# Kernel optimization log

Hardware: AMD Instinct MI355X
Metric: run time of the kernel (lower is better)

Reference implementation:

```python
import jax, jax.numpy as jnp
import numpy as np

B, D, S = 128, 256, 512
K, H, NCLS = 50, 256, 2
THRES = 0.3  # conceptshap threshold


def _l2norm(x, axis):
    n = jnp.sqrt(jnp.sum(x * x, axis=axis, keepdims=True))
    return x / jnp.maximum(n, 1e-12)


def setup_inputs() -> dict:
    key = jax.random.key(0)
    ks = jax.random.split(key, 6)
    return {
        "f_input": jax.random.normal(ks[0], (B, D, S), dtype=jnp.float32),
        "targets": jax.random.uniform(ks[1], (B,), dtype=jnp.float32),
        "topic_vector": jax.random.uniform(ks[2], (D, K), minval=-0.5, maxval=0.5, dtype=jnp.float32),
        "rec_vector_1": jax.random.uniform(ks[3], (K, H), minval=-0.5, maxval=0.5, dtype=jnp.float32),
        "rec_vector_2": jax.random.uniform(ks[4], (H, D), minval=-0.5, maxval=0.5, dtype=jnp.float32),
        "Wc": jax.random.normal(ks[5], (D, NCLS), dtype=jnp.float32) * 0.05,
        "bc": jnp.zeros((NCLS,), dtype=jnp.float32),
        "causal": 0,
    }


def reference(f_input, targets, topic_vector, rec_vector_1, rec_vector_2, Wc, bc, causal):
    # text path (n=3), model_name != 'transformer' -> swap to [B, S, D]
    x = jnp.swapaxes(f_input, 1, 2)                # [B, S, D]
    x_n = _l2norm(x, axis=-1)                      # F.normalize(dim=n-1)
    tv_n = _l2norm(topic_vector, axis=0)           # [D, K], column-normalized

    topic_prob = jnp.einsum('bsd,dk->bsk', x, tv_n)      # [B, S, K]
    topic_prob_n = jnp.einsum('bsd,dk->bsk', x_n, tv_n)  # [B, S, K]

    # conceptshap: no softmax, hard threshold mask
    mask = (topic_prob_n > THRES).astype(topic_prob.dtype)
    topic_prob_am = topic_prob * mask
    topic_prob_sum = jnp.sum(topic_prob_am, axis=-1, keepdims=True) + 0.001
    topic_prob_nn = topic_prob_am / (topic_prob_sum + 1e-8)

    rec_layer_1 = jax.nn.relu(jnp.einsum('bsk,kh->bsh', topic_prob_nn, rec_vector_1))
    rec_layer_2 = jnp.einsum('bsh,hd->bsd', rec_layer_1, rec_vector_2)  # [B, S, D]

    ae_loss = jnp.mean((x_n - rec_layer_2) ** 2)

    rec_out = jnp.swapaxes(rec_layer_2, 1, 2)      # back to [B, D, S]
    # frozen classifier: mean over seq + linear head
    pred = jnp.mean(rec_out, axis=-1) @ Wc + bc    # [B, NCLS]

    # concept_sim: mean of per-concept top-(B//4) similarity scores, negated
    res = topic_prob_n.reshape(-1, K).T            # [K, B*S]
    topv, _ = jax.lax.top_k(res, B // 4)
    concept_sim = -jnp.mean(topv)

    concept_far = jnp.mean(tv_n.T @ tv_n - jnp.eye(K, dtype=tv_n.dtype))

    return (pred, jnp.float32(0.0), concept_sim, concept_far, topic_prob_nn, ae_loss)
```

## Files before the change

### kernel.cpp

```cpp
#include <hip/hip_runtime.h>
#include <math.h>

#define BB 128
#define DD 256
#define SS 512
#define KK 50
#define HH 256
#define TS 128
#define NTILES (BB * SS / TS)
#define NBLK (NTILES * 2)
#define BS (BB * SS)

#define CHUNK 1024
#define NCH (BS / CHUNK)
#define NCHBLK (KK * NCH / 4)
#define TOPK 32
#define MAXSURV 512
#define NSUB (TS / 16)

#define TVN_OFF 0
#define TVNT_OFF (TVN_OFF + DD * KK)
#define TPNT_OFF (TVNT_OFF + KK * DD)
#define PREDACC_OFF (TPNT_OFF + KK * BS)
#define AE_OFF (PREDACC_OFF + BB * DD)
#define SIM_OFF (AE_OFF + 1)
#define CNT_OFF (AE_OFF + 2)
#define SIMD_OFF (AE_OFF + 3)
#define TFLAG_OFF (AE_OFF + 4)
#define TCNT_OFF (TFLAG_OFF + NTILES)
#define NZERO (BB * DD + 4 + 2 * NTILES)
#define LIST_OFF (TCNT_OFF + NTILES)
#define CAND_OFF (LIST_OFF + MAXSURV)

#define OUT_NN_OFF 259
#define OUT_AE_IDX (OUT_NN_OFF + KK * BS)

__device__ __forceinline__ unsigned fkey(float f) {
  unsigned u = __float_as_uint(f);
  return (u & 0x80000000u) ? ~u : (u | 0x80000000u);
}
__device__ __forceinline__ float keyval(unsigned T) {
  unsigned u = (T & 0x80000000u) ? (T & 0x7FFFFFFFu) : ~T;
  return __uint_as_float(u);
}

__global__ __launch_bounds__(256) void tvn_kernel(const float* __restrict__ tv,
                                                  float* __restrict__ tvn,
                                                  float* __restrict__ tvnT,
                                                  float* __restrict__ zbase) {
  __shared__ float red[256];
  const int k = blockIdx.x, t = threadIdx.x;
  {
    const int gid = k * 256 + t;
    for (int i = gid; i < NZERO; i += KK * 256) zbase[i] = 0.0f;
  }
  float v = tv[t * KK + k];
  red[t] = v * v;
  __syncthreads();
  for (int off = 128; off > 0; off >>= 1) {
    if (t < off) red[t] += red[t + off];
    __syncthreads();
  }
  float inv = 1.0f / fmaxf(sqrtf(red[0]), 1e-12f);
  const float nv = v * inv;
  tvn[t * KK + k] = nv;
  tvnT[k * DD + t] = nv;
}

__global__ __launch_bounds__(256, 4) void main_kernel(
    const float* __restrict__ f_input, const float* __restrict__ tvnT,
    float* __restrict__ out_nn, float* __restrict__ tpn_t,
    float* __restrict__ ae_acc, int* __restrict__ surv_cnt,
    int* __restrict__ surv_list, int* __restrict__ tile_flag,
    int* __restrict__ tile_cnt) {
  __shared__ int wflag[4];
  __shared__ int decision;

  const int blk = blockIdx.x;
  const int tile = blk >> 1;
  const int half = blk & 1;
  const int b = tile >> 2;
  const int s0 = (tile & 3) * TS;
  const int t = threadIdx.x;
  const int lane = t & 63;
  const int wid = t >> 6;
  const int kb = __builtin_amdgcn_readfirstlane(half * 4 + wid);

  const float* tvk[7];
  bool kval[7];
  #pragma unroll
  for (int j = 0; j < 7; ++j) {
    const int k = kb + 8 * j;
    kval[j] = (k < KK);
    tvk[j] = tvnT + (size_t)(kval[j] ? k : (KK - 1)) * DD;
  }

  const float* xp = f_input + (size_t)b * DD * SS + s0 + 2 * lane;

  float acc0[7], acc1[7];
  #pragma unroll
  for (int j = 0; j < 7; ++j) { acc0[j] = 0.0f; acc1[j] = 0.0f; }

  float2 xb[2][4];
  #pragma unroll
  for (int i = 0; i < 4; ++i) xb[0][i] = *(const float2*)(xp + (size_t)i * SS);

  float s2_0 = 0.0f, s2_1 = 0.0f;
  int buf = 0;
  for (int part = 0; part < 8; ++part) {
    float p0 = 0.0f, p1 = 0.0f;
    #pragma unroll
    for (int dd = 0; dd < 32; dd += 4) {
      const int d0 = part * 32 + dd;
      const int dn = (d0 + 4 < DD) ? (d0 + 4) : 0;
      #pragma unroll
      for (int i = 0; i < 4; ++i) xb[buf ^ 1][i] = *(const float2*)(xp + (size_t)(dn + i) * SS);
      const float2 xa = xb[buf][0], xc2 = xb[buf][1], xc3 = xb[buf][2], xc4 = xb[buf][3];
      p0 += xa.x * xa.x; p0 += xc2.x * xc2.x; p0 += xc3.x * xc3.x; p0 += xc4.x * xc4.x;
      p1 += xa.y * xa.y; p1 += xc2.y * xc2.y; p1 += xc3.y * xc3.y; p1 += xc4.y * xc4.y;
      #pragma unroll
      for (int j = 0; j < 7; ++j) {
        const float4 tq = *(const float4*)(tvk[j] + d0);
        acc0[j] += xa.x * tq.x; acc0[j] += xc2.x * tq.y;
        acc0[j] += xc3.x * tq.z; acc0[j] += xc4.x * tq.w;
        acc1[j] += xa.y * tq.x; acc1[j] += xc2.y * tq.y;
        acc1[j] += xc3.y * tq.z; acc1[j] += xc4.y * tq.w;
      }
      buf ^= 1;
    }
    s2_0 = (part == 0) ? p0 : (s2_0 + p0);
    s2_1 = (part == 0) ? p1 : (s2_1 + p1);
  }
  const float i0 = 1.0f / fmaxf(sqrtf(s2_0), 1e-12f);
  const float i1 = 1.0f / fmaxf(sqrtf(s2_1), 1e-12f);

  bool m = false;
  const size_t gs = (size_t)b * SS + s0 + 2 * lane;
  #pragma unroll
  for (int j = 0; j < 7; ++j) {
    if (kval[j]) {
      const int k = kb + 8 * j;
      float2 o;
      o.x = acc0[j] * i0;
      o.y = acc1[j] * i1;
      *(float2*)(tpn_t + (size_t)k * BS + gs) = o;
      m = m | (o.x > 0.3f) | (o.y > 0.3f);
    }
  }

  const int w = __any((int)m);
  if (lane == 0) wflag[wid] = w;
  __syncthreads();
  const int blockAny = wflag[0] | wflag[1] | wflag[2] | wflag[3];

  if (t == 0) {
    const int old = atomicOr(&tile_flag[tile], blockAny);
    const int done = atomicAdd(&tile_cnt[tile], 1);
    int dec = 0;
    if (done == 1) {
      const int fl = old | blockAny;
      if (fl) {
        const int idx = atomicAdd(surv_cnt, 1);
        if (idx < MAXSURV) surv_list[idx] = tile;
      } else {
        atomicAdd(ae_acc, (float)TS);
        dec = 1;
      }
    }
    decision = dec;
  }
  __syncthreads();
  if (decision) {
    float* ob = out_nn + ((size_t)b * SS + s0) * KK;
    for (int p2 = t; p2 < TS * KK; p2 += 256) ob[p2] = 0.0f;
  }
}

__global__ __launch_bounds__(256) void chunk_surv_kernel(
    const float* __restrict__ tpn_t, float* __restrict__ cand,
    const float* __restrict__ f_input, const float* __restrict__ rec1,
    const float* __restrict__ rec2, const int* __restrict__ surv_cnt,
    const int* __restrict__ surv_list, float* __restrict__ out_nn,
    float* __restrict__ predacc, float* __restrict__ ae_acc) {
  __shared__ __align__(16) float NNk[KK * 20];
  __shared__ __align__(16) float R1t[HH * 20];
  __shared__ float nprt[16][17];
  __shared__ float nrm[16], invn[16];
  __shared__ float pm[8 * DD];
  __shared__ float red4[4];

  const int t = threadIdx.x;
  const int lane = t & 63, wid = t >> 6;

  if (blockIdx.x < NCHBLK) {
    const int gchunk = blockIdx.x * 4 + wid;
    const int k = gchunk >> 6;
    const int c = gchunk & (NCH - 1);
    const float* row = tpn_t + (size_t)k * BS + c * CHUNK;

    float v[16];
    unsigned key[16];
    #pragma unroll
    for (int j = 0; j < 16; ++j) {
      v[j] = row[lane + j * 64];
      key[j] = fkey(v[j]);
    }
    unsigned T = 0;
    for (int bit = 31; bit >= 0; --bit) {
      const unsigned ct = T | (1u << bit);
      int cnt = 0;
      #pragma unroll
      for (int j = 0; j < 16; ++j) cnt += (key[j] >= ct) ? 1 : 0;
      #pragma unroll
      for (int off = 1; off < 64; off <<= 1) cnt += __shfl_xor(cnt, off);
      if (cnt >= TOPK) T = ct;
    }
    int cg = 0;
    #pragma unroll
    for (int j = 0; j < 16; ++j) cg += (key[j] > T) ? 1 : 0;
    int incl = cg;
    #pragma unroll
    for (int off = 1; off < 64; off <<= 1) {
      int y = __shfl_up(incl, off);
      if (lane >= off) incl += y;
    }
    const int excl = incl - cg;
    const int total_gt = __shfl(incl, 63);

    float* cb = cand + (size_t)gchunk * TOPK;
    int pos = excl;
    #pragma unroll
    for (int j = 0; j < 16; ++j) {
      if (key[j] > T) cb[pos++] = v[j];
    }
    if (lane < TOPK - total_gt) cb[total_gt + lane] = keyval(T);
    return;
  }

  const int bid = blockIdx.x - NCHBLK;
  int cnt = *surv_cnt;
  if (cnt > MAXSURV) cnt = MAXSURV;
  const int ntask = NSUB * cnt;

  for (int task = bid; task < ntask; task += 64) {
    const int tile = surv_list[task / NSUB];
    const int q = task % NSUB;
    const int b = tile >> 2;
    const int s0 = (tile & 3) * TS + q * 16;
    const float* fb = f_input + (size_t)b * DD * SS;
    const size_t gs0 = (size_t)b * SS + s0;

    for (int p = t; p < KK * 16; p += 256) {
      const int k = p >> 4, ss = p & 15;
      NNk[k * 20 + ss] = tpn_t[(size_t)k * BS + gs0 + ss];
    }
    {
      const int ss = t & 15, part = t >> 4;
      const float* xc = fb + (size_t)(part * 16) * SS + s0 + ss;
      float p = 0.0f;
      #pragma unroll
      for (int i = 0; i < 16; ++i) {
        const float v = xc[(size_t)i * SS];
        p += v * v;
      }
      nprt[part][ss] = p;
    }
    __syncthreads();
    if (t < 16) {
      float s2 = 0.0f;
      #pragma unroll
      for (int i = 0; i < 16; ++i) s2 += nprt[i][t];
      const float n = fmaxf(sqrtf(s2), 1e-12f);
      nrm[t] = n;
      invn[t] = 1.0f / n;
      float sm = 0.0f;
      for (int k = 0; k < KK; ++k) {
        const float tpn = NNk[k * 20 + t];
        sm += (tpn > 0.3f) ? tpn * n : 0.0f;
      }
      const float idv = 1.0f / (sm + 0.001f + 1e-8f);
      for (int k = 0; k < KK; ++k) {
        const float tpn = NNk[k * 20 + t];
        NNk[k * 20 + t] = (tpn > 0.3f) ? tpn * n * idv : 0.0f;
      }
    }
    __syncthreads();

    for (int p = t; p < 16 * KK; p += 256) {
      const int ss = p / KK, k = p - ss * KK;
      out_nn[(gs0 + ss) * KK + k] = NNk[k * 20 + ss];
    }

    {
      float a[16];
      #pragma unroll
      for (int i = 0; i < 16; ++i) a[i] = 0.0f;
      #pragma unroll 2
      for (int k = 0; k < KK; ++k) {
        const float r = rec1[k * HH + t];
        const float4* np = (const float4*)&NNk[k * 20];
        #pragma unroll
        for (int qq = 0; qq < 4; ++qq) {
          const float4 nv = np[qq];
          a[qq * 4 + 0] += nv.x * r;
          a[qq * 4 + 1] += nv.y * r;
          a[qq * 4 + 2] += nv.z * r;
          a[qq * 4 + 3] += nv.w * r;
        }
      }
      #pragma unroll
      for (int i = 0; i < 16; ++i) R1t[t * 20 + i] = fmaxf(a[i], 0.0f);
    }
    __syncthreads();

    const int tx = t & 31, ty = t >> 5;
    const int d0 = tx * 8, sb = ty * 2;
    float c2[2][8];
    #pragma unroll
    for (int i = 0; i < 2; ++i)
      #pragma unroll
      for (int j = 0; j < 8; ++j) c2[i][j] = 0.0f;
    for (int h0 = 0; h0 < HH; h0 += 8) {
      float4 B0[8], B1[8];
      #pragma unroll
      for (int u = 0; u < 8; ++u) {
        B0[u] = *(const float4*)(rec2 + (h0 + u) * DD + d0);
        B1[u] = *(const float4*)(rec2 + (h0 + u) * DD + d0 + 4);
      }
      #pragma unroll
      for (int u = 0; u < 8; ++u) {
        const float2 a01 = *(const float2*)(&R1t[(h0 + u) * 20 + sb]);
        const float bv[8] = {B0[u].x, B0[u].y, B0[u].z, B0[u].w,
                             B1[u].x, B1[u].y, B1[u].z, B1[u].w};
        #pragma unroll
        for (int j = 0; j < 8; ++j) {
          c2[0][j] += a01.x * bv[j];
          c2[1][j] += a01.y * bv[j];
        }
      }
    }
    #pragma unroll
    for (int j = 0; j < 8; ++j) pm[ty * DD + d0 + j] = c2[0][j] + c2[1][j];
    __syncthreads();
    {
      float sum = 0.0f;
      #pragma unroll
      for (int r = 0; r < 8; ++r) sum += pm[r * DD + t];
      atomicAdd(&predacc[(size_t)b * DD + t], sum);
    }
    float e = 0.0f;
    #pragma unroll
    for (int j = 0; j < 8; ++j) {
      #pragma unroll
      for (int i = 0; i < 2; ++i) {
        const float x = fb[(size_t)(d0 + j) * SS + s0 + sb + i];
        const float diff = x * invn[sb + i] - c2[i][j];
        e += diff * diff;
      }
    }
    #pragma unroll
    for (int off = 1; off < 64; off <<= 1) e += __shfl_xor(e, off);
    if (lane == 0) red4[wid] = e;
    __syncthreads();
    if (t == 0) atomicAdd(ae_acc, red4[0] + red4[1] + red4[2] + red4[3]);
    __syncthreads();
  }
}

__global__ __launch_bounds__(256) void merge_finalize_kernel(
    const float* __restrict__ cand, const float* __restrict__ predacc,
    const float* __restrict__ Wc, const float* __restrict__ bc,
    const float* __restrict__ ae_acc, float* __restrict__ sim_acc,
    unsigned* __restrict__ sim_done, const float* __restrict__ tvn,
    float* __restrict__ out) {
  __shared__ float r0[256], r1[256];
  const int blk = blockIdx.x;
  const int t = threadIdx.x;

  if (blk >= BB) {
    if (t < 64) {
      const int k = blk - BB;
      const int lane = t;
      const float* row = cand + (size_t)k * (NCH * TOPK);
      float v[32];
      unsigned key[32];
      #pragma unroll
      for (int j = 0; j < 32; ++j) {
        v[j] = row[lane + j * 64];
        key[j] = fkey(v[j]);
      }
      unsigned T = 0;
      for (int bit = 31; bit >= 0; --bit) {
        const unsigned ct = T | (1u << bit);
        int cnt = 0;
        #pragma unroll
        for (int j = 0; j < 32; ++j) cnt += (key[j] >= ct) ? 1 : 0;
        #pragma unroll
        for (int off = 1; off < 64; off <<= 1) cnt += __shfl_xor(cnt, off);
        if (cnt >= TOPK) T = ct;
      }
      float s = 0.0f;
      int cgt = 0;
      #pragma unroll
      for (int j = 0; j < 32; ++j) {
        if (key[j] > T) { s += v[j]; cgt++; }
      }
      #pragma unroll
      for (int off = 1; off < 64; off <<= 1) {
        s += __shfl_xor(s, off);
        cgt += __shfl_xor(cgt, off);
      }
      if (lane == 0) {
        atomicAdd(sim_acc, s + (float)(TOPK - cgt) * keyval(T));
        __threadfence();
        const unsigned c = atomicAdd(sim_done, 1u);
        if (c == KK - 1) {
          __threadfence();
          const float tot = atomicAdd(sim_acc, 0.0f);
          out[257] = -tot * (1.0f / (float)(KK * TOPK));
        }
      }
    }
    return;
  }

  const float s = predacc[(size_t)blk * DD + t];
  r0[t] = s * Wc[t * 2 + 0];
  r1[t] = s * Wc[t * 2 + 1];
  __syncthreads();
  for (int off = 128; off > 0; off >>= 1) {
    if (t < off) { r0[t] += r0[t + off]; r1[t] += r1[t + off]; }
    __syncthreads();
  }
  if (t == 0) {
    out[blk * 2 + 0] = r0[0] * (1.0f / (float)SS) + bc[0];
    out[blk * 2 + 1] = r1[0] * (1.0f / (float)SS) + bc[1];
    if (blk == 0) {
      out[256] = 0.0f;
      out[OUT_AE_IDX] = (*ae_acc) * (1.0f / ((float)BB * (float)SS * (float)DD));
    }
  }
  if (blk == 0) {
    __syncthreads();
    float rs = 0.0f;
    for (int k = 0; k < KK; ++k) rs += tvn[t * KK + k];
    r0[t] = rs * rs;
    __syncthreads();
    for (int off = 128; off > 0; off >>= 1) {
      if (t < off) r0[t] += r0[t + off];
      __syncthreads();
    }
    if (t == 0) out[258] = (r0[0] - (float)KK) / ((float)KK * (float)KK);
  }
}

extern "C" void kernel_launch(void* const* d_in, const int* in_sizes, int n_in,
                              void* d_out, int out_size, void* d_ws, size_t ws_size,
                              hipStream_t stream) {
  (void)in_sizes; (void)n_in; (void)out_size; (void)ws_size;
  const float* f_input = (const float*)d_in[0];
  const float* tv = (const float*)d_in[2];
  const float* rec1 = (const float*)d_in[3];
  const float* rec2 = (const float*)d_in[4];
  const float* Wc = (const float*)d_in[5];
  const float* bc = (const float*)d_in[6];

  float* out = (float*)d_out;
  float* ws = (float*)d_ws;
  float* tvn = ws + TVN_OFF;
  float* tvnT = ws + TVNT_OFF;
  float* tpn_t = ws + TPNT_OFF;
  float* predacc = ws + PREDACC_OFF;
  float* ae_acc = ws + AE_OFF;
  float* sim_acc = ws + SIM_OFF;
  int* surv_cnt = (int*)(ws + CNT_OFF);
  unsigned* sim_done = (unsigned*)(ws + SIMD_OFF);
  int* tile_flag = (int*)(ws + TFLAG_OFF);
  int* tile_cnt = (int*)(ws + TCNT_OFF);
  int* surv_list = (int*)(ws + LIST_OFF);
  float* cand = ws + CAND_OFF;

  tvn_kernel<<<KK, 256, 0, stream>>>(tv, tvn, tvnT, predacc);
  main_kernel<<<NBLK, 256, 0, stream>>>(f_input, tvnT, out + OUT_NN_OFF, tpn_t,
                                        ae_acc, surv_cnt, surv_list,
                                        tile_flag, tile_cnt);
  chunk_surv_kernel<<<NCHBLK + 64, 256, 0, stream>>>(
      tpn_t, cand, f_input, rec1, rec2, surv_cnt, surv_list,
      out + OUT_NN_OFF, predacc, ae_acc);
  merge_finalize_kernel<<<BB + KK, 256, 0, stream>>>(
      cand, predacc, Wc, bc, ae_acc, sim_acc, sim_done, tvn, out);
}
```

Baseline: 225.8 us.

## Fuse four kernel launches into one cooperative kernel with grid syncs

```diff
diff --git a/kernel.cpp b/kernel.cpp
--- a/kernel.cpp
+++ b/kernel.cpp
@@ -1,4 +1,5 @@
 #include <hip/hip_runtime.h>
+#include <hip/hip_cooperative_groups.h>
 #include <math.h>
 
 #define BB 128
@@ -44,6 +45,423 @@
   return __uint_as_float(u);
 }
 
+union __align__(16) AllShared {
+  float red[512];
+  struct { int wflag[4]; int decision; } mn;
+  struct {
+    float NNk[KK * 20];
+    float R1t[HH * 20];
+    float nprt[16][17];
+    float nrm[16];
+    float invn[16];
+    float pm[8 * DD];
+    float red4[4];
+  } sv;
+};
+
+__global__ __launch_bounds__(256, 4) void fused_kernel(
+    const float* __restrict__ f_input, const float* __restrict__ tv,
+    const float* __restrict__ rec1, const float* __restrict__ rec2,
+    const float* __restrict__ Wc, const float* __restrict__ bc,
+    float* __restrict__ out, float* __restrict__ ws) {
+  __shared__ AllShared sh;
+
+  float* tvn = ws + TVN_OFF;
+  float* tvnT = ws + TVNT_OFF;
+  float* tpn_t = ws + TPNT_OFF;
+  float* predacc = ws + PREDACC_OFF;
+  float* ae_acc = ws + AE_OFF;
+  float* sim_acc = ws + SIM_OFF;
+  int* surv_cnt = (int*)(ws + CNT_OFF);
+  unsigned* sim_done = (unsigned*)(ws + SIMD_OFF);
+  int* tile_flag = (int*)(ws + TFLAG_OFF);
+  int* tile_cnt = (int*)(ws + TCNT_OFF);
+  int* surv_list = (int*)(ws + LIST_OFF);
+  float* cand = ws + CAND_OFF;
+  float* out_nn = out + OUT_NN_OFF;
+
+  const int t = threadIdx.x;
+  const int lane = t & 63, wid = t >> 6;
+
+  {
+    const int gid = blockIdx.x * 256 + t;
+    if (gid < NZERO) predacc[gid] = 0.0f;
+    if (blockIdx.x < KK) {
+      const int k = blockIdx.x;
+      float v = tv[t * KK + k];
+      sh.red[t] = v * v;
+      __syncthreads();
+      for (int off = 128; off > 0; off >>= 1) {
+        if (t < off) sh.red[t] += sh.red[t + off];
+        __syncthreads();
+      }
+      const float inv = 1.0f / fmaxf(sqrtf(sh.red[0]), 1e-12f);
+      const float nv = v * inv;
+      tvn[t * KK + k] = nv;
+      tvnT[k * DD + t] = nv;
+    }
+  }
+  cooperative_groups::this_grid().sync();
+
+  {
+    const int blk = blockIdx.x;
+    const int tile = blk >> 1;
+    const int half = blk & 1;
+    const int b = tile >> 2;
+    const int s0 = (tile & 3) * TS;
+    const int kb = __builtin_amdgcn_readfirstlane(half * 4 + wid);
+
+    const float* tvk[7];
+    bool kval[7];
+    #pragma unroll
+    for (int j = 0; j < 7; ++j) {
+      const int k = kb + 8 * j;
+      kval[j] = (k < KK);
+      tvk[j] = tvnT + (size_t)(kval[j] ? k : (KK - 1)) * DD;
+    }
+
+    const float* xp = f_input + (size_t)b * DD * SS + s0 + 2 * lane;
+
+    float acc0[7], acc1[7];
+    #pragma unroll
+    for (int j = 0; j < 7; ++j) { acc0[j] = 0.0f; acc1[j] = 0.0f; }
+
+    float2 xb[2][8];
+    #pragma unroll
+    for (int i = 0; i < 8; ++i) xb[0][i] = *(const float2*)(xp + (size_t)i * SS);
+
+    float s2_0 = 0.0f, s2_1 = 0.0f;
+    int buf = 0;
+    for (int part = 0; part < 8; ++part) {
+      float p0 = 0.0f, p1 = 0.0f;
+      #pragma unroll
+      for (int dd = 0; dd < 32; dd += 8) {
+        const int d0 = part * 32 + dd;
+        const int dn = (d0 + 8 < DD) ? (d0 + 8) : 0;
+        #pragma unroll
+        for (int i = 0; i < 8; ++i) xb[buf ^ 1][i] = *(const float2*)(xp + (size_t)(dn + i) * SS);
+        #pragma unroll
+        for (int g = 0; g < 2; ++g) {
+          const float2 xa = xb[buf][4 * g + 0], xc2 = xb[buf][4 * g + 1],
+                       xc3 = xb[buf][4 * g + 2], xc4 = xb[buf][4 * g + 3];
+          p0 += xa.x * xa.x; p0 += xc2.x * xc2.x; p0 += xc3.x * xc3.x; p0 += xc4.x * xc4.x;
+          p1 += xa.y * xa.y; p1 += xc2.y * xc2.y; p1 += xc3.y * xc3.y; p1 += xc4.y * xc4.y;
+          #pragma unroll
+          for (int j = 0; j < 7; ++j) {
+            const float4 tq = *(const float4*)(tvk[j] + d0 + 4 * g);
+            acc0[j] += xa.x * tq.x; acc0[j] += xc2.x * tq.y;
+            acc0[j] += xc3.x * tq.z; acc0[j] += xc4.x * tq.w;
+            acc1[j] += xa.y * tq.x; acc1[j] += xc2.y * tq.y;
+            acc1[j] += xc3.y * tq.z; acc1[j] += xc4.y * tq.w;
+          }
+        }
+        buf ^= 1;
+      }
+      s2_0 = (part == 0) ? p0 : (s2_0 + p0);
+      s2_1 = (part == 0) ? p1 : (s2_1 + p1);
+    }
+    const float i0 = 1.0f / fmaxf(sqrtf(s2_0), 1e-12f);
+    const float i1 = 1.0f / fmaxf(sqrtf(s2_1), 1e-12f);
+
+    bool m = false;
+    const size_t gs = (size_t)b * SS + s0 + 2 * lane;
+    #pragma unroll
+    for (int j = 0; j < 7; ++j) {
+      if (kval[j]) {
+        const int k = kb + 8 * j;
+        float2 o;
+        o.x = acc0[j] * i0;
+        o.y = acc1[j] * i1;
+        *(float2*)(tpn_t + (size_t)k * BS + gs) = o;
+        m = m | (o.x > 0.3f) | (o.y > 0.3f);
+      }
+    }
+
+    const int w = __any((int)m);
+    if (lane == 0) sh.mn.wflag[wid] = w;
+    __syncthreads();
+    const int blockAny = sh.mn.wflag[0] | sh.mn.wflag[1] | sh.mn.wflag[2] | sh.mn.wflag[3];
+
+    if (t == 0) {
+      const int old = atomicOr(&tile_flag[tile], blockAny);
+      const int done = atomicAdd(&tile_cnt[tile], 1);
+      int dec = 0;
+      if (done == 1) {
+        const int fl = old | blockAny;
+        if (fl) {
+          const int idx = atomicAdd(surv_cnt, 1);
+          if (idx < MAXSURV) surv_list[idx] = tile;
+        } else {
+          atomicAdd(ae_acc, (float)TS);
+          dec = 1;
+        }
+      }
+      sh.mn.decision = dec;
+    }
+    __syncthreads();
+    if (sh.mn.decision) {
+      float* ob = out_nn + ((size_t)b * SS + s0) * KK;
+      for (int p2 = t; p2 < TS * KK; p2 += 256) ob[p2] = 0.0f;
+    }
+  }
+  cooperative_groups::this_grid().sync();
+
+  if (blockIdx.x < NCHBLK) {
+    const int gchunk = blockIdx.x * 4 + wid;
+    const int k = gchunk >> 6;
+    const int c = gchunk & (NCH - 1);
+    const float* row = tpn_t + (size_t)k * BS + c * CHUNK;
+
+    float v[16];
+    unsigned key[16];
+    #pragma unroll
+    for (int j = 0; j < 16; ++j) {
+      v[j] = row[lane + j * 64];
+      key[j] = fkey(v[j]);
+    }
+    unsigned T = 0;
+    for (int bit = 31; bit >= 0; --bit) {
+      const unsigned ct = T | (1u << bit);
+      int cnt = 0;
+      #pragma unroll
+      for (int j = 0; j < 16; ++j) cnt += (key[j] >= ct) ? 1 : 0;
+      #pragma unroll
+      for (int off = 1; off < 64; off <<= 1) cnt += __shfl_xor(cnt, off);
+      if (cnt >= TOPK) T = ct;
+    }
+    int cge = 0;
+    #pragma unroll
+    for (int j = 0; j < 16; ++j) cge += (key[j] > T) ? 1 : 0;
+    int incl = cge;
+    #pragma unroll
+    for (int off = 1; off < 64; off <<= 1) {
+      int y = __shfl_up(incl, off);
+      if (lane >= off) incl += y;
+    }
+    const int excl = incl - cge;
+    const int total_gt = __shfl(incl, 63);
+
+    float* cb = cand + (size_t)gchunk * TOPK;
+    int pos = excl;
+    #pragma unroll
+    for (int j = 0; j < 16; ++j) {
+      if (key[j] > T) cb[pos++] = v[j];
+    }
+    if (lane < TOPK - total_gt) cb[total_gt + lane] = keyval(T);
+  } else if (blockIdx.x < NCHBLK + 64) {
+    float* NNk = sh.sv.NNk;
+    float* R1t = sh.sv.R1t;
+    const int bid = blockIdx.x - NCHBLK;
+    int cnt = *surv_cnt;
+    if (cnt > MAXSURV) cnt = MAXSURV;
+    const int ntask = NSUB * cnt;
+
+    for (int task = bid; task < ntask; task += 64) {
+      const int tile = surv_list[task / NSUB];
+      const int q = task % NSUB;
+      const int b = tile >> 2;
+      const int s0 = (tile & 3) * TS + q * 16;
+      const float* fb = f_input + (size_t)b * DD * SS;
+      const size_t gs0 = (size_t)b * SS + s0;
+
+      for (int p = t; p < KK * 16; p += 256) {
+        const int k = p >> 4, ss = p & 15;
+        NNk[k * 20 + ss] = tpn_t[(size_t)k * BS + gs0 + ss];
+      }
+      {
+        const int ss = t & 15, part = t >> 4;
+        const float* xc = fb + (size_t)(part * 16) * SS + s0 + ss;
+        float p = 0.0f;
+        #pragma unroll
+        for (int i = 0; i < 16; ++i) {
+          const float v = xc[(size_t)i * SS];
+          p += v * v;
+        }
+        sh.sv.nprt[part][ss] = p;
+      }
+      __syncthreads();
+      if (t < 16) {
+        float s2 = 0.0f;
+        #pragma unroll
+        for (int i = 0; i < 16; ++i) s2 += sh.sv.nprt[i][t];
+        const float n = fmaxf(sqrtf(s2), 1e-12f);
+        sh.sv.nrm[t] = n;
+        sh.sv.invn[t] = 1.0f / n;
+        float sm = 0.0f;
+        for (int k = 0; k < KK; ++k) {
+          const float tpn = NNk[k * 20 + t];
+          sm += (tpn > 0.3f) ? tpn * n : 0.0f;
+        }
+        const float idv = 1.0f / (sm + 0.001f + 1e-8f);
+        for (int k = 0; k < KK; ++k) {
+          const float tpn = NNk[k * 20 + t];
+          NNk[k * 20 + t] = (tpn > 0.3f) ? tpn * n * idv : 0.0f;
+        }
+      }
+      __syncthreads();
+
+      for (int p = t; p < 16 * KK; p += 256) {
+        const int ss = p / KK, k = p - ss * KK;
+        out_nn[(gs0 + ss) * KK + k] = NNk[k * 20 + ss];
+      }
+
+      {
+        float a[16];
+        #pragma unroll
+        for (int i = 0; i < 16; ++i) a[i] = 0.0f;
+        #pragma unroll 2
+        for (int k = 0; k < KK; ++k) {
+          const float r = rec1[k * HH + t];
+          const float4* np = (const float4*)&NNk[k * 20];
+          #pragma unroll
+          for (int qq = 0; qq < 4; ++qq) {
+            const float4 nv = np[qq];
+            a[qq * 4 + 0] += nv.x * r;
+            a[qq * 4 + 1] += nv.y * r;
+            a[qq * 4 + 2] += nv.z * r;
+            a[qq * 4 + 3] += nv.w * r;
+          }
+        }
+        #pragma unroll
+        for (int i = 0; i < 16; ++i) R1t[t * 20 + i] = fmaxf(a[i], 0.0f);
+      }
+      __syncthreads();
+
+      const int tx = t & 31, ty = t >> 5;
+      const int d0 = tx * 8, sb = ty * 2;
+      float c2[2][8];
+      #pragma unroll
+      for (int i = 0; i < 2; ++i)
+        #pragma unroll
+        for (int j = 0; j < 8; ++j) c2[i][j] = 0.0f;
+      for (int h0 = 0; h0 < HH; h0 += 8) {
+        float4 B0[8], B1[8];
+        #pragma unroll
+        for (int u = 0; u < 8; ++u) {
+          B0[u] = *(const float4*)(rec2 + (h0 + u) * DD + d0);
+          B1[u] = *(const float4*)(rec2 + (h0 + u) * DD + d0 + 4);
+        }
+        #pragma unroll
+        for (int u = 0; u < 8; ++u) {
+          const float2 a01 = *(const float2*)(&R1t[(h0 + u) * 20 + sb]);
+          const float bv[8] = {B0[u].x, B0[u].y, B0[u].z, B0[u].w,
+                               B1[u].x, B1[u].y, B1[u].z, B1[u].w};
+          #pragma unroll
+          for (int j = 0; j < 8; ++j) {
+            c2[0][j] += a01.x * bv[j];
+            c2[1][j] += a01.y * bv[j];
+          }
+        }
+      }
+      #pragma unroll
+      for (int j = 0; j < 8; ++j) sh.sv.pm[ty * DD + d0 + j] = c2[0][j] + c2[1][j];
+      __syncthreads();
+      {
+        float sum = 0.0f;
+        #pragma unroll
+        for (int r = 0; r < 8; ++r) sum += sh.sv.pm[r * DD + t];
+        atomicAdd(&predacc[(size_t)b * DD + t], sum);
+      }
+      float e = 0.0f;
+      #pragma unroll
+      for (int j = 0; j < 8; ++j) {
+        #pragma unroll
+        for (int i = 0; i < 2; ++i) {
+          const float x = fb[(size_t)(d0 + j) * SS + s0 + sb + i];
+          const float diff = x * sh.sv.invn[sb + i] - c2[i][j];
+          e += diff * diff;
+        }
+      }
+      #pragma unroll
+      for (int off = 1; off < 64; off <<= 1) e += __shfl_xor(e, off);
+      if (lane == 0) sh.sv.red4[wid] = e;
+      __syncthreads();
+      if (t == 0) atomicAdd(ae_acc, sh.sv.red4[0] + sh.sv.red4[1] + sh.sv.red4[2] + sh.sv.red4[3]);
+      __syncthreads();
+    }
+  }
+  cooperative_groups::this_grid().sync();
+
+  {
+    const int blk = blockIdx.x;
+    if (blk >= BB && blk < BB + KK) {
+      if (t < 64) {
+        const int k = blk - BB;
+        const float* row = cand + (size_t)k * (NCH * TOPK);
+        float v[32];
+        unsigned key[32];
+        #pragma unroll
+        for (int j = 0; j < 32; ++j) {
+          v[j] = row[t + j * 64];
+          key[j] = fkey(v[j]);
+        }
+        unsigned T = 0;
+        for (int bit = 31; bit >= 0; --bit) {
+          const unsigned ct = T | (1u << bit);
+          int cnt = 0;
+          #pragma unroll
+          for (int j = 0; j < 32; ++j) cnt += (key[j] >= ct) ? 1 : 0;
+          #pragma unroll
+          for (int off = 1; off < 64; off <<= 1) cnt += __shfl_xor(cnt, off);
+          if (cnt >= TOPK) T = ct;
+        }
+        float s = 0.0f;
+        int cgt = 0;
+        #pragma unroll
+        for (int j = 0; j < 32; ++j) {
+          if (key[j] > T) { s += v[j]; cgt++; }
+        }
+        #pragma unroll
+        for (int off = 1; off < 64; off <<= 1) {
+          s += __shfl_xor(s, off);
+          cgt += __shfl_xor(cgt, off);
+        }
+        if (t == 0) {
+          atomicAdd(sim_acc, s + (float)(TOPK - cgt) * keyval(T));
+          __threadfence();
+          const unsigned c = atomicAdd(sim_done, 1u);
+          if (c == KK - 1) {
+            __threadfence();
+            const float tot = atomicAdd(sim_acc, 0.0f);
+            out[257] = -tot * (1.0f / (float)(KK * TOPK));
+          }
+        }
+      }
+    } else if (blk < BB) {
+      float* r0 = sh.red;
+      float* r1 = sh.red + 256;
+      const float s = predacc[(size_t)blk * DD + t];
+      r0[t] = s * Wc[t * 2 + 0];
+      r1[t] = s * Wc[t * 2 + 1];
+      __syncthreads();
+      for (int off = 128; off > 0; off >>= 1) {
+        if (t < off) { r0[t] += r0[t + off]; r1[t] += r1[t + off]; }
+        __syncthreads();
+      }
+      if (t == 0) {
+        out[blk * 2 + 0] = r0[0] * (1.0f / (float)SS) + bc[0];
+        out[blk * 2 + 1] = r1[0] * (1.0f / (float)SS) + bc[1];
+        if (blk == 0) {
+          out[256] = 0.0f;
+          out[OUT_AE_IDX] = (*ae_acc) * (1.0f / ((float)BB * (float)SS * (float)DD));
+        }
+      }
+      if (blk == 0) {
+        __syncthreads();
+        float rs = 0.0f;
+        for (int k = 0; k < KK; ++k) rs += tvn[t * KK + k];
+        r0[t] = rs * rs;
+        __syncthreads();
+        for (int off = 128; off > 0; off >>= 1) {
+          if (t < off) r0[t] += r0[t + off];
+          __syncthreads();
+        }
+        if (t == 0) out[258] = (r0[0] - (float)KK) / ((float)KK * (float)KK);
+      }
+    }
+  }
+}
+
 __global__ __launch_bounds__(256) void tvn_kernel(const float* __restrict__ tv,
                                                   float* __restrict__ tvn,
                                                   float* __restrict__ tvnT,
@@ -215,16 +633,16 @@
       for (int off = 1; off < 64; off <<= 1) cnt += __shfl_xor(cnt, off);
       if (cnt >= TOPK) T = ct;
     }
-    int cg = 0;
-    #pragma unroll
-    for (int j = 0; j < 16; ++j) cg += (key[j] > T) ? 1 : 0;
-    int incl = cg;
+    int cge = 0;
+    #pragma unroll
+    for (int j = 0; j < 16; ++j) cge += (key[j] > T) ? 1 : 0;
+    int incl = cge;
     #pragma unroll
     for (int off = 1; off < 64; off <<= 1) {
       int y = __shfl_up(incl, off);
       if (lane >= off) incl += y;
     }
-    const int excl = incl - cg;
+    const int excl = incl - cge;
     const int total_gt = __shfl(incl, 63);
 
     float* cb = cand + (size_t)gchunk * TOPK;
@@ -467,26 +885,34 @@
 
   float* out = (float*)d_out;
   float* ws = (float*)d_ws;
-  float* tvn = ws + TVN_OFF;
-  float* tvnT = ws + TVNT_OFF;
-  float* tpn_t = ws + TPNT_OFF;
-  float* predacc = ws + PREDACC_OFF;
-  float* ae_acc = ws + AE_OFF;
-  float* sim_acc = ws + SIM_OFF;
-  int* surv_cnt = (int*)(ws + CNT_OFF);
-  unsigned* sim_done = (unsigned*)(ws + SIMD_OFF);
-  int* tile_flag = (int*)(ws + TFLAG_OFF);
-  int* tile_cnt = (int*)(ws + TCNT_OFF);
-  int* surv_list = (int*)(ws + LIST_OFF);
-  float* cand = ws + CAND_OFF;
-
-  tvn_kernel<<<KK, 256, 0, stream>>>(tv, tvn, tvnT, predacc);
-  main_kernel<<<NBLK, 256, 0, stream>>>(f_input, tvnT, out + OUT_NN_OFF, tpn_t,
-                                        ae_acc, surv_cnt, surv_list,
-                                        tile_flag, tile_cnt);
-  chunk_surv_kernel<<<NCHBLK + 64, 256, 0, stream>>>(
-      tpn_t, cand, f_input, rec1, rec2, surv_cnt, surv_list,
-      out + OUT_NN_OFF, predacc, ae_acc);
-  merge_finalize_kernel<<<BB + KK, 256, 0, stream>>>(
-      cand, predacc, Wc, bc, ae_acc, sim_acc, sim_done, tvn, out);
+
+  void* args[] = {(void*)&f_input, (void*)&tv, (void*)&rec1, (void*)&rec2,
+                  (void*)&Wc, (void*)&bc, (void*)&out, (void*)&ws};
+  const hipError_t err = hipLaunchCooperativeKernel(
+      (const void*)fused_kernel, dim3(NBLK), dim3(256), args, 0u, stream);
+
+  if (err != hipSuccess) {
+    float* tvn = ws + TVN_OFF;
+    float* tvnT = ws + TVNT_OFF;
+    float* tpn_t = ws + TPNT_OFF;
+    float* predacc = ws + PREDACC_OFF;
+    float* ae_acc = ws + AE_OFF;
+    float* sim_acc = ws + SIM_OFF;
+    int* surv_cnt = (int*)(ws + CNT_OFF);
+    unsigned* sim_done = (unsigned*)(ws + SIMD_OFF);
+    int* tile_flag = (int*)(ws + TFLAG_OFF);
+    int* tile_cnt = (int*)(ws + TCNT_OFF);
+    int* surv_list = (int*)(ws + LIST_OFF);
+    float* cand = ws + CAND_OFF;
+
+    tvn_kernel<<<KK, 256, 0, stream>>>(tv, tvn, tvnT, predacc);
+    main_kernel<<<NBLK, 256, 0, stream>>>(f_input, tvnT, out + OUT_NN_OFF, tpn_t,
+                                          ae_acc, surv_cnt, surv_list,
+                                          tile_flag, tile_cnt);
+    chunk_surv_kernel<<<NCHBLK + 64, 256, 0, stream>>>(
+        tpn_t, cand, f_input, rec1, rec2, surv_cnt, surv_list,
+        out + OUT_NN_OFF, predacc, ae_acc);
+    merge_finalize_kernel<<<BB + KK, 256, 0, stream>>>(
+        cand, predacc, Wc, bc, ae_acc, sim_acc, sim_done, tvn, out);
+  }
 }
```

New measurement: 687.1 us. 3.04x slower.

## Stage input tile through LDS with double buffering and split sequence across blocks

Applied to the files above, without the earlier changes.

```diff
diff --git a/kernel.cpp b/kernel.cpp
--- a/kernel.cpp
+++ b/kernel.cpp
@@ -73,6 +73,7 @@
     float* __restrict__ ae_acc, int* __restrict__ surv_cnt,
     int* __restrict__ surv_list, int* __restrict__ tile_flag,
     int* __restrict__ tile_cnt) {
+  __shared__ __align__(16) float xs[2][32 * 64];
   __shared__ int wflag[4];
   __shared__ int decision;
 
@@ -80,71 +81,99 @@
   const int tile = blk >> 1;
   const int half = blk & 1;
   const int b = tile >> 2;
-  const int s0 = (tile & 3) * TS;
+  const int s0t = (tile & 3) * TS;
+  const int s0 = s0t + half * 64;
   const int t = threadIdx.x;
   const int lane = t & 63;
   const int wid = t >> 6;
-  const int kb = __builtin_amdgcn_readfirstlane(half * 4 + wid);
-
-  const float* tvk[7];
-  bool kval[7];
+  const int kb = __builtin_amdgcn_readfirstlane(wid);
+
+  const float* tvk[13];
+  bool kval[13];
   #pragma unroll
-  for (int j = 0; j < 7; ++j) {
-    const int k = kb + 8 * j;
+  for (int j = 0; j < 13; ++j) {
+    const int k = kb + 4 * j;
     kval[j] = (k < KK);
     tvk[j] = tvnT + (size_t)(kval[j] ? k : (KK - 1)) * DD;
   }
 
-  const float* xp = f_input + (size_t)b * DD * SS + s0 + 2 * lane;
-
-  float acc0[7], acc1[7];
+  const float* fb = f_input + (size_t)b * DD * SS;
+  const int srow = wid * 8 + (lane >> 4);
+  const int scol = (lane & 15) * 4;
+  const float* gst = fb + (size_t)srow * SS + s0 + scol;
+  const int ls0 = srow * 64 + scol;
+
+  float acc[13];
   #pragma unroll
-  for (int j = 0; j < 7; ++j) { acc0[j] = 0.0f; acc1[j] = 0.0f; }
-
-  float2 xb[2][4];
+  for (int j = 0; j < 13; ++j) acc[j] = 0.0f;
+
+  float4 Ra0, Ra1, Rb0, Rb1;
+  Rb0 = *(const float4*)(gst + (size_t)0 * SS);
+  Rb1 = *(const float4*)(gst + (size_t)4 * SS);
+  *(float4*)&xs[0][ls0] = Rb0;
+  *(float4*)&xs[0][ls0 + 4 * 64] = Rb1;
+  Ra0 = *(const float4*)(gst + (size_t)(32 + 0) * SS);
+  Ra1 = *(const float4*)(gst + (size_t)(32 + 4) * SS);
+  __syncthreads();
+
+  float s2 = 0.0f;
+
+#define COMPUTE_PART(bf, p)                                                    \
+  {                                                                            \
+    float pp = 0.0f;                                                           \
+    _Pragma("unroll")                                                          \
+    for (int dd = 0; dd < 32; dd += 4) {                                       \
+      const int d0 = (p) * 32 + dd;                                            \
+      const float x0 = xs[bf][(dd + 0) * 64 + lane];                           \
+      const float x1 = xs[bf][(dd + 1) * 64 + lane];                           \
+      const float x2 = xs[bf][(dd + 2) * 64 + lane];                           \
+      const float x3 = xs[bf][(dd + 3) * 64 + lane];                           \
+            \
+      pp += x0 * x0; pp += x1 * x1; pp += x2 * x2; pp += x3 * x3;              \
+      _Pragma("unroll")                                                        \
+      for (int j = 0; j < 13; ++j) {                                           \
+        const float4 tq = *(const float4*)(tvk[j] + d0);   \
+        acc[j] += x0 * tq.x; acc[j] += x1 * tq.y;                              \
+        acc[j] += x2 * tq.z; acc[j] += x3 * tq.w;                              \
+      }                                                                        \
+    }                                                                          \
+    s2 = ((p) == 0) ? pp : (s2 + pp);                                          \
+  }
+
+  for (int cc = 0; cc < 4; ++cc) {
+    const int c0 = 2 * cc;
+    if (cc < 3) {
+      Rb0 = *(const float4*)(gst + (size_t)((c0 + 2) * 32 + 0) * SS);
+      Rb1 = *(const float4*)(gst + (size_t)((c0 + 2) * 32 + 4) * SS);
+    }
+    COMPUTE_PART(0, c0);
+    *(float4*)&xs[1][ls0] = Ra0;
+    *(float4*)&xs[1][ls0 + 4 * 64] = Ra1;
+    __syncthreads();
+    if (cc < 3) {
+      Ra0 = *(const float4*)(gst + (size_t)((c0 + 3) * 32 + 0) * SS);
+      Ra1 = *(const float4*)(gst + (size_t)((c0 + 3) * 32 + 4) * SS);
+    }
+    COMPUTE_PART(1, c0 + 1);
+    if (cc < 3) {
+      *(float4*)&xs[0][ls0] = Rb0;
+      *(float4*)&xs[0][ls0 + 4 * 64] = Rb1;
+      __syncthreads();
+    }
+  }
+#undef COMPUTE_PART
+
+  const float i0 = 1.0f / fmaxf(sqrtf(s2), 1e-12f);
+
+  bool m = false;
+  const size_t gs = (size_t)b * SS + s0 + lane;
   #pragma unroll
-  for (int i = 0; i < 4; ++i) xb[0][i] = *(const float2*)(xp + (size_t)i * SS);
-
-  float s2_0 = 0.0f, s2_1 = 0.0f;
-  int buf = 0;
-  for (int part = 0; part < 8; ++part) {
-    float p0 = 0.0f, p1 = 0.0f;
-    #pragma unroll
-    for (int dd = 0; dd < 32; dd += 4) {
-      const int d0 = part * 32 + dd;
-      const int dn = (d0 + 4 < DD) ? (d0 + 4) : 0;
-      #pragma unroll
-      for (int i = 0; i < 4; ++i) xb[buf ^ 1][i] = *(const float2*)(xp + (size_t)(dn + i) * SS);
-      const float2 xa = xb[buf][0], xc2 = xb[buf][1], xc3 = xb[buf][2], xc4 = xb[buf][3];
-      p0 += xa.x * xa.x; p0 += xc2.x * xc2.x; p0 += xc3.x * xc3.x; p0 += xc4.x * xc4.x;
-      p1 += xa.y * xa.y; p1 += xc2.y * xc2.y; p1 += xc3.y * xc3.y; p1 += xc4.y * xc4.y;
-      #pragma unroll
-      for (int j = 0; j < 7; ++j) {
-        const float4 tq = *(const float4*)(tvk[j] + d0);
-        acc0[j] += xa.x * tq.x; acc0[j] += xc2.x * tq.y;
-        acc0[j] += xc3.x * tq.z; acc0[j] += xc4.x * tq.w;
-        acc1[j] += xa.y * tq.x; acc1[j] += xc2.y * tq.y;
-        acc1[j] += xc3.y * tq.z; acc1[j] += xc4.y * tq.w;
-      }
-      buf ^= 1;
-    }
-    s2_0 = (part == 0) ? p0 : (s2_0 + p0);
-    s2_1 = (part == 0) ? p1 : (s2_1 + p1);
-  }
-  const float i0 = 1.0f / fmaxf(sqrtf(s2_0), 1e-12f);
-  const float i1 = 1.0f / fmaxf(sqrtf(s2_1), 1e-12f);
-
-  bool m = false;
-  const size_t gs = (size_t)b * SS + s0 + 2 * lane;
-  #pragma unroll
-  for (int j = 0; j < 7; ++j) {
+  for (int j = 0; j < 13; ++j) {
     if (kval[j]) {
-      const int k = kb + 8 * j;
-      float2 o;
-      o.x = acc0[j] * i0;
-      o.y = acc1[j] * i1;
-      *(float2*)(tpn_t + (size_t)k * BS + gs) = o;
-      m = m | (o.x > 0.3f) | (o.y > 0.3f);
+      const int k = kb + 4 * j;
+      const float o = acc[j] * i0;
+      tpn_t[(size_t)k * BS + gs] = o;
+      m = m | (o > 0.3f);
     }
   }
 
@@ -171,7 +200,7 @@
   }
   __syncthreads();
   if (decision) {
-    float* ob = out_nn + ((size_t)b * SS + s0) * KK;
+    float* ob = out_nn + ((size_t)b * SS + s0t) * KK;
     for (int p2 = t; p2 < TS * KK; p2 += 256) ob[p2] = 0.0f;
   }
 }
```

After: 283.6 us. +25.6%, slower.
